# Kernel tuning notes

Hardware: AMD Instinct MI355X
Metric: run time of the kernel (lower is better)

The kernel has to match this reference:

```python
import jax, jax.numpy as jnp
import numpy as np

TEMPERATURE = 0.5
EPS = 1e-8  # matches F.cosine_similarity eps clamp


def setup_inputs() -> dict:
    key = jax.random.key(0)
    k1, k2 = jax.random.split(key)
    logits = jax.random.normal(k1, (8192, 256), dtype=jnp.float32)
    label = jax.random.randint(k2, (8192,), 0, 10, dtype=jnp.int64)
    return {"logits": logits, "label": label}


def reference(logits, label):
    n = label.shape[0]
    # pairwise cosine similarity via normalize + GEMM (same math as the
    # broadcasted F.cosine_similarity, without the O(n^2 d) intermediate)
    norms = jnp.maximum(jnp.linalg.norm(logits, axis=1, keepdims=True), EPS)
    xn = logits / norms                       # [n, d]
    sim_matrix = xn @ xn.T                    # [n, n]

    eye = jnp.eye(n, dtype=sim_matrix.dtype)
    mask = (label[:, None] == label[None, :]).astype(sim_matrix.dtype)  # same-label (incl. diag)

    e = jnp.exp(sim_matrix / TEMPERATURE) * (1.0 - eye)  # zero diagonal
    sim = mask * e                            # same-label positives
    no_sim_sum = jnp.sum(e - sim, axis=1)     # [n] row sums of different-label terms
    sim_sum = sim + no_sim_sum[:, None]       # denominator per entry
    ratio = sim / sim_sum

    # zeros (different-label entries) get +1 via (1 - mask), diagonal gets +1 via eye -> -log(1) = 0
    loss_mat = -jnp.log((1.0 - mask) + ratio + eye)
    return jnp.sum(loss_mat) / (2 * n)
```

## Files before the change

### kernel.cpp

```cpp
#include <hip/hip_runtime.h>
#include <cstdint>
#include <cstddef>

typedef float  f32x4  __attribute__((ext_vector_type(4)));
typedef long long i64;
typedef unsigned char uchar;

#define N_ROWS 8192
#define KDIM   256
#define TEMP_INV 2.0f
#define LOG2E  1.4426950408889634f
#define EXPC   (TEMP_INV * LOG2E)

#define AS1 __attribute__((address_space(1)))
#define AS3 __attribute__((address_space(3)))

__global__ __launch_bounds__(256) void prep(const float* __restrict__ logits,
        const int* __restrict__ label, uchar* __restrict__ xn8,
        int* __restrict__ perm, int* __restrict__ labelPerm,
        int* __restrict__ classStart, int* __restrict__ cumTiles)
{
    __shared__ int lcnt[256][10];
    __shared__ int cstart[11];
    __shared__ int ccount[10];
    const int tid = threadIdx.x;
    const int bid = blockIdx.x;

    if (bid < 2048) {
        const int p = bid * 4 + (tid >> 6);
        const int lane = tid & 63;
        float4 v = reinterpret_cast<const float4*>(logits + (size_t)p * KDIM)[lane];
        float ss = v.x*v.x + v.y*v.y + v.z*v.z + v.w*v.w;
        #pragma unroll
        for (int off = 32; off >= 1; off >>= 1) ss += __shfl_xor(ss, off, 64);
        float inv = 1.0f / fmaxf(sqrtf(ss), 1e-8f);
        int pk = __builtin_amdgcn_cvt_pk_fp8_f32(v.x * inv, v.y * inv, 0, false);
        pk     = __builtin_amdgcn_cvt_pk_fp8_f32(v.z * inv, v.w * inv, pk, true);
        reinterpret_cast<unsigned int*>(xn8 + (size_t)p * KDIM)[lane] = (unsigned int)pk;
        return;
    }

    const int wave = tid >> 6, lane = tid & 63;
    const int beg = tid * 32, end = beg + 32;
    int loc[10] = {0,0,0,0,0,0,0,0,0,0};
    for (int i = beg; i < end; ++i) {
        int c = label[i]; c = (c < 0) ? 0 : (c > 9 ? 9 : c);
        loc[c]++;
    }
    #pragma unroll
    for (int c = 0; c < 10; ++c) lcnt[tid][c] = loc[c];
    __syncthreads();

    for (int c = wave; c < 10; c += 4) {
        int s0 = lcnt[lane*4+0][c], s1 = lcnt[lane*4+1][c];
        int s2 = lcnt[lane*4+2][c], s3 = lcnt[lane*4+3][c];
        int tot = s0 + s1 + s2 + s3;
        int incl = tot;
        #pragma unroll
        for (int d = 1; d < 64; d <<= 1) {
            int up = __shfl_up(incl, d, 64);
            if (lane >= d) incl += up;
        }
        int excl = incl - tot;
        lcnt[lane*4+0][c] = excl;
        lcnt[lane*4+1][c] = excl + s0;
        lcnt[lane*4+2][c] = excl + s0 + s1;
        lcnt[lane*4+3][c] = excl + s0 + s1 + s2;
        if (lane == 63) ccount[c] = incl;
    }
    __syncthreads();

    if (tid == 0) {
        int run = 0, runT = 0;
        for (int c = 0; c < 10; ++c) {
            cstart[c] = run; classStart[c] = run;
            int tpc = (ccount[c] + 127) >> 7;
            cumTiles[c] = runT;
            run  += ccount[c];
            runT += tpc * (tpc + 1) / 2;
        }
        cstart[10] = run; classStart[10] = run; cumTiles[10] = runT;
    }
    __syncthreads();

    int ofs[10];
    #pragma unroll
    for (int c = 0; c < 10; ++c) ofs[c] = lcnt[tid][c];
    for (int i = beg; i < end; ++i) {
        int c = label[i]; c = (c < 0) ? 0 : (c > 9 ? 9 : c);
        int pos = cstart[c] + ofs[c]++;
        perm[pos] = i;
        labelPerm[pos] = c;
    }
}

__device__ __forceinline__ void stage_oneshot(const uchar* __restrict__ xn8,
        const int* __restrict__ perm, int rowBase, int colBase,
        uchar* As, uchar* Bs, int tid)
{
    const int t4 = tid >> 4;
    const int ch = (tid & 15) ^ t4;
    #pragma unroll
    for (int i = 0; i < 8; ++i) {
        const int row = i * 16 + t4;
        int rA = rowBase + row; if (rA > N_ROWS - 1) rA = N_ROWS - 1;
        int rB = colBase + row; if (rB > N_ROWS - 1) rB = N_ROWS - 1;
        const int lds_off = (i * 256 + tid) * 16;
        const uchar* gA = xn8 + (size_t)perm[rA] * KDIM + ch * 16;
        const uchar* gB = xn8 + (size_t)perm[rB] * KDIM + ch * 16;
        __builtin_amdgcn_global_load_lds((const AS1 void*)gA, (AS3 void*)(As + lds_off), 16, 0, 0);
        __builtin_amdgcn_global_load_lds((const AS1 void*)gB, (AS3 void*)(Bs + lds_off), 16, 0, 0);
    }
}

__device__ __forceinline__ void mfma_oneshot(const uchar* As, const uchar* Bs,
        f32x4 (&acc)[4][4], int wave, int lane)
{
    const int wr = wave >> 1, wc = wave & 1;
    const int lrow = lane & 15, kgrp = lane >> 4;
    const int ch2 = kgrp >> 1, half8 = (kgrp & 1) * 8;
    #pragma unroll
    for (int s = 0; s < 8; ++s) {
        const int c16 = s * 2 + ch2;
        i64 a[4], b[4];
        #pragma unroll
        for (int mi = 0; mi < 4; ++mi) {
            const int row = wr*64 + mi*16 + lrow;
            a[mi] = *reinterpret_cast<const i64*>(As + (size_t)row * 256 + ((c16 ^ lrow) * 16) + half8);
        }
        #pragma unroll
        for (int ni = 0; ni < 4; ++ni) {
            const int row = wc*64 + ni*16 + lrow;
            b[ni] = *reinterpret_cast<const i64*>(Bs + (size_t)row * 256 + ((c16 ^ lrow) * 16) + half8);
        }
        #pragma unroll
        for (int mi = 0; mi < 4; ++mi)
            #pragma unroll
            for (int ni = 0; ni < 4; ++ni)
                acc[mi][ni] = __builtin_amdgcn_mfma_f32_16x16x32_fp8_fp8(a[mi], b[ni], acc[mi][ni], 0, 0, 0);
    }
}

__global__ __launch_bounds__(256, 2) void phase1_gemm(const uchar* __restrict__ xn8,
        const int* __restrict__ perm, const int* __restrict__ labelPerm,
        float* __restrict__ pD)
{
    __shared__ __align__(16) char pool[65536];
    uchar* As = (uchar*)(pool);
    uchar* Bs = (uchar*)(pool + 32768);
    float* rowD = (float*)pool;
    float* colD = (float*)(pool + 16384);
    __shared__ int labLDS[256];

    const int tid = threadIdx.x;
    const int wave = tid >> 6, lane = tid & 63;

    int t = blockIdx.x, bi = 0;
    while (t >= 64 - bi) { t -= 64 - bi; ++bi; }
    const int bj = bi + t;
    const bool isDiag = (bi == bj);
    const int rowBase = bi * 128, colBase = bj * 128;

    if (labelPerm[rowBase] == labelPerm[colBase + 127]) {
        if (tid < 128)       pD[(size_t)bj * N_ROWS + rowBase + tid] = 0.f;
        else if (!isDiag)    pD[(size_t)bi * N_ROWS + colBase + tid - 128] = 0.f;
        return;
    }

    stage_oneshot(xn8, perm, rowBase, colBase, As, Bs, tid);
    labLDS[tid] = labelPerm[(tid < 128) ? (rowBase + tid) : (colBase + tid - 128)];
    __syncthreads();

    f32x4 acc[4][4] = {};
    mfma_oneshot(As, Bs, acc, wave, lane);
    __syncthreads();

    const int wr = wave >> 1, wc = wave & 1;
    const int lrow = lane & 15, lgrp = lane >> 4;
    float colAcc[4] = {0.f, 0.f, 0.f, 0.f};
    #pragma unroll
    for (int mi = 0; mi < 4; ++mi) {
        #pragma unroll
        for (int reg = 0; reg < 4; ++reg) {
            const int tr = wr * 64 + mi * 16 + lgrp * 4 + reg;
            const int rl = labLDS[tr];
            float rowAcc = 0.f;
            #pragma unroll
            for (int ni = 0; ni < 4; ++ni) {
                const int tc = wc * 64 + ni * 16 + lrow;
                float e = __builtin_amdgcn_exp2f(acc[mi][ni][reg] * EXPC);
                float ed = (rl != labLDS[128 + tc]) ? e : 0.f;
                rowAcc += ed;
                colAcc[ni] += ed;
            }
            rowD[tr * 32 + wc * 16 + lrow] = rowAcc;
        }
    }
    if (!isDiag) {
        #pragma unroll
        for (int ni = 0; ni < 4; ++ni) {
            const int tc = wc * 64 + ni * 16 + lrow;
            colD[tc * 8 + wr * 4 + lgrp] = colAcc[ni];
        }
    }
    __syncthreads();

    if (tid < 128) {
        const float* p = rowD + tid * 32;
        float s = 0.f;
        #pragma unroll
        for (int k = 0; k < 8; ++k) {
            f32x4 v = *reinterpret_cast<const f32x4*>(p + k * 4);
            s += v[0] + v[1] + v[2] + v[3];
        }
        pD[(size_t)bj * N_ROWS + rowBase + tid] = s;
    } else if (!isDiag) {
        const int c2 = tid - 128;
        const float* p = colD + c2 * 8;
        f32x4 v0 = *reinterpret_cast<const f32x4*>(p);
        f32x4 v1 = *reinterpret_cast<const f32x4*>(p + 4);
        pD[(size_t)bi * N_ROWS + colBase + c2] =
            v0[0] + v0[1] + v0[2] + v0[3] + v1[0] + v1[1] + v1[2] + v1[3];
    }
}

__global__ __launch_bounds__(256, 2) void phase3_loss(const uchar* __restrict__ xn8,
        const int* __restrict__ perm, const float* __restrict__ pD,
        const int* __restrict__ classStart, const int* __restrict__ cumTiles,
        float* __restrict__ partial)
{
    __shared__ __align__(16) char pool[65536];
    uchar* As = (uchar*)(pool);
    uchar* Bs = (uchar*)(pool + 32768);
    __shared__ float redF[256];
    __shared__ float DarrH[256];
    __shared__ float DarrR[128];
    __shared__ float DarrC[128];
    __shared__ int   meta[22];

    const int tid = threadIdx.x;
    const int wave = tid >> 6, lane = tid & 63;

    if (tid < 11) { meta[tid] = classStart[tid]; meta[11 + tid] = cumTiles[tid]; }
    __syncthreads();
    const int nTiles = meta[11 + 10];

    float tileSum = 0.f;
    for (int b = blockIdx.x; b < nTiles; b += 512) {
        __syncthreads();

        int c = 0;
        while (c < 9 && b >= meta[11 + c + 1]) ++c;
        const int s = meta[c], e = meta[c + 1];
        const int nc = e - s;
        const int tps = (nc + 127) >> 7;
        int lt = b - meta[11 + c];
        int ti = 0;
        while (lt >= tps - ti) { lt -= tps - ti; ++ti; }
        const int tj = ti + lt;
        const bool isDiagT = (ti == tj);
        const int rowBase = s + ti * 128, colBase = s + tj * 128;

        stage_oneshot(xn8, perm, rowBase, colBase, As, Bs, tid);

        {
            int r = rowBase + (tid & 127); if (r > N_ROWS - 1) r = N_ROWS - 1;
            const int half = tid >> 7;
            float d = 0.f;
            #pragma unroll 4
            for (int sl = half * 32; sl < half * 32 + 32; ++sl)
                d += pD[(size_t)sl * N_ROWS + r];
            DarrH[(tid & 127) * 2 + half] = d;
        }
        __syncthreads();
        if (tid < 128) DarrR[tid] = DarrH[tid * 2] + DarrH[tid * 2 + 1];
        __syncthreads();
        if (!isDiagT) {
            int r = colBase + (tid & 127); if (r > N_ROWS - 1) r = N_ROWS - 1;
            const int half = tid >> 7;
            float d = 0.f;
            #pragma unroll 4
            for (int sl = half * 32; sl < half * 32 + 32; ++sl)
                d += pD[(size_t)sl * N_ROWS + r];
            DarrH[(tid & 127) * 2 + half] = d;
            __syncthreads();
            if (tid < 128) DarrC[tid] = DarrH[tid * 2] + DarrH[tid * 2 + 1];
        }
        __syncthreads();

        f32x4 acc[4][4] = {};
        mfma_oneshot(As, Bs, acc, wave, lane);

        const int wr = wave >> 1, wc = wave & 1;
        const int lrow = lane & 15, lgrp = lane >> 4;
        #pragma unroll
        for (int mi = 0; mi < 4; ++mi) {
            #pragma unroll
            for (int reg = 0; reg < 4; ++reg) {
                const int tr = wr * 64 + mi * 16 + lgrp * 4 + reg;
                const int r = rowBase + tr;
                if (r < e) {
                    const float Dr = DarrR[tr];
                    #pragma unroll
                    for (int ni = 0; ni < 4; ++ni) {
                        const int tc = wc * 64 + ni * 16 + lrow;
                        const int cg = colBase + tc;
                        if (cg < e) {
                            float sim = acc[mi][ni][reg];
                            float ev = __builtin_amdgcn_exp2f(sim * EXPC);
                            if (isDiagT) {
                                if (cg != r)
                                    tileSum += __logf(ev + Dr) - TEMP_INV * sim;
                            } else {
                                tileSum += __logf(ev + Dr) + __logf(ev + DarrC[tc])
                                         - 2.0f * TEMP_INV * sim;
                            }
                        }
                    }
                }
            }
        }
    }

    __syncthreads();
    redF[tid] = tileSum;
    __syncthreads();
    for (int st = 128; st > 0; st >>= 1) {
        if (tid < st) redF[tid] += redF[tid + st];
        __syncthreads();
    }
    if (tid == 0) partial[blockIdx.x] = redF[0];
}

__global__ void phase4_final(const float* __restrict__ partial, float* __restrict__ out)
{
    __shared__ float red[256];
    const int tid = threadIdx.x;
    float s = partial[tid] + partial[tid + 256];
    red[tid] = s;
    __syncthreads();
    for (int st = 128; st > 0; st >>= 1) {
        if (tid < st) red[tid] += red[tid + st];
        __syncthreads();
    }
    if (tid == 0) out[0] = red[0] * (1.0f / 16384.0f);
}

extern "C" void kernel_launch(void* const* d_in, const int* in_sizes, int n_in,
                              void* d_out, int out_size, void* d_ws, size_t ws_size,
                              hipStream_t stream)
{
    const float* logits = (const float*)d_in[0];
    const int*   label  = (const int*)d_in[1];
    float* out = (float*)d_out;

    char* ws = (char*)d_ws;
    uchar*  xn8       = (uchar*)(ws);
    float*  pD        = (float*)(ws + (2u << 20));
    int*    perm      = (int*)(ws + (4u << 20));
    int*    labelPerm = (int*)(ws + (4u << 20) + (32u << 10));
    int*    classStart= (int*)(ws + (4u << 20) + (64u << 10));
    int*    cumTiles  = (int*)(ws + (4u << 20) + (64u << 10) + 256);
    float*  partial   = (float*)(ws + (4u << 20) + (128u << 10));

    hipLaunchKernelGGL(prep, dim3(2049), dim3(256), 0, stream,
                       logits, label, xn8, perm, labelPerm, classStart, cumTiles);
    hipLaunchKernelGGL(phase1_gemm, dim3(2080), dim3(256), 0, stream,
                       xn8, perm, labelPerm, pD);
    hipLaunchKernelGGL(phase3_loss, dim3(512), dim3(256), 0, stream,
                       xn8, perm, pD, classStart, cumTiles, partial);
    hipLaunchKernelGGL(phase4_final, dim3(1), dim3(256), 0, stream,
                       partial, out);
}
```

Before: 67.97 us.

## Use 512-thread blocks in phase1 GEMM and coalesce label scan in prep

phase1_gemm now runs 8 waves per 128x128 tile, each computing a 64x32 sub-tile, so each wave holds fewer accumulators and there are more waves per tile to hide latency. Row and column partial sums are reduced with cross-lane shuffles before being written to LDS, which shrinks the final reduction. The prep kernel reads labels strided by thread (coalesced) into registers once, instead of each thread reading a contiguous 32-element run twice. The risk is that 512-thread blocks with 64KB of LDS limit how many blocks fit per CU, and the extra shuffles add instructions. The permutation order within each class also changes.

```diff
diff --git a/kernel.cpp b/kernel.cpp
--- a/kernel.cpp
+++ b/kernel.cpp
@@ -41,12 +41,15 @@
     }
 
     const int wave = tid >> 6, lane = tid & 63;
-    const int beg = tid * 32, end = beg + 32;
+    int lab[32];
+    #pragma unroll
+    for (int j = 0; j < 32; ++j) {
+        int c = label[tid + j * 256];
+        lab[j] = (c < 0) ? 0 : (c > 9 ? 9 : c);
+    }
     int loc[10] = {0,0,0,0,0,0,0,0,0,0};
-    for (int i = beg; i < end; ++i) {
-        int c = label[i]; c = (c < 0) ? 0 : (c > 9 ? 9 : c);
-        loc[c]++;
-    }
+    #pragma unroll
+    for (int j = 0; j < 32; ++j) loc[lab[j]]++;
     #pragma unroll
     for (int c = 0; c < 10; ++c) lcnt[tid][c] = loc[c];
     __syncthreads();
@@ -86,11 +89,125 @@
     int ofs[10];
     #pragma unroll
     for (int c = 0; c < 10; ++c) ofs[c] = lcnt[tid][c];
-    for (int i = beg; i < end; ++i) {
-        int c = label[i]; c = (c < 0) ? 0 : (c > 9 ? 9 : c);
+    #pragma unroll
+    for (int j = 0; j < 32; ++j) {
+        int c = lab[j];
         int pos = cstart[c] + ofs[c]++;
-        perm[pos] = i;
+        perm[pos] = tid + j * 256;
         labelPerm[pos] = c;
+    }
+}
+
+__global__ __launch_bounds__(512, 4) void phase1_gemm(const uchar* __restrict__ xn8,
+        const int* __restrict__ perm, const int* __restrict__ labelPerm,
+        float* __restrict__ pD)
+{
+    __shared__ __align__(16) char pool[65536];
+    uchar* As = (uchar*)(pool);
+    uchar* Bs = (uchar*)(pool + 32768);
+    float* rowD = (float*)pool;
+    float* colD = (float*)(pool + 32768);
+    __shared__ int labLDS[256];
+
+    const int tid = threadIdx.x;
+    const int wave = tid >> 6, lane = tid & 63;
+
+    int t = blockIdx.x, bi = 0;
+    while (t >= 64 - bi) { t -= 64 - bi; ++bi; }
+    const int bj = bi + t;
+    const bool isDiag = (bi == bj);
+    const int rowBase = bi * 128, colBase = bj * 128;
+
+    if (labelPerm[rowBase] == labelPerm[colBase + 127]) {
+        if (tid < 128)                    pD[(size_t)bj * N_ROWS + rowBase + tid] = 0.f;
+        else if (tid < 256 && !isDiag)    pD[(size_t)bi * N_ROWS + colBase + tid - 128] = 0.f;
+        return;
+    }
+
+    {
+        const int t4 = (tid >> 4) & 15;
+        const int ch = (tid & 15) ^ t4;
+        #pragma unroll
+        for (int i = 0; i < 4; ++i) {
+            const int ci = i * 512 + tid;
+            const int row = ci >> 4;
+            const int lds_off = ci * 16;
+            const uchar* gA = xn8 + (size_t)perm[rowBase + row] * KDIM + ch * 16;
+            const uchar* gB = xn8 + (size_t)perm[colBase + row] * KDIM + ch * 16;
+            __builtin_amdgcn_global_load_lds((const AS1 void*)gA, (AS3 void*)(As + lds_off), 16, 0, 0);
+            __builtin_amdgcn_global_load_lds((const AS1 void*)gB, (AS3 void*)(Bs + lds_off), 16, 0, 0);
+        }
+    }
+    if (tid < 256)
+        labLDS[tid] = labelPerm[(tid < 128) ? (rowBase + tid) : (colBase + tid - 128)];
+    __syncthreads();
+
+    const int wr = wave >> 2, wc = wave & 3;
+    const int lrow = lane & 15, kgrp = lane >> 4;
+    const int ch2 = kgrp >> 1, half8 = (kgrp & 1) * 8;
+    f32x4 acc[4][2] = {};
+    #pragma unroll
+    for (int s = 0; s < 8; ++s) {
+        const int c16 = s * 2 + ch2;
+        i64 a[4], b[2];
+        #pragma unroll
+        for (int mi = 0; mi < 4; ++mi) {
+            const int row = wr*64 + mi*16 + lrow;
+            a[mi] = *reinterpret_cast<const i64*>(As + (size_t)row * 256 + ((c16 ^ lrow) * 16) + half8);
+        }
+        #pragma unroll
+        for (int ni = 0; ni < 2; ++ni) {
+            const int row = wc*32 + ni*16 + lrow;
+            b[ni] = *reinterpret_cast<const i64*>(Bs + (size_t)row * 256 + ((c16 ^ lrow) * 16) + half8);
+        }
+        #pragma unroll
+        for (int mi = 0; mi < 4; ++mi)
+            #pragma unroll
+            for (int ni = 0; ni < 2; ++ni)
+                acc[mi][ni] = __builtin_amdgcn_mfma_f32_16x16x32_fp8_fp8(a[mi], b[ni], acc[mi][ni], 0, 0, 0);
+    }
+    __syncthreads();
+
+    const int lgrp = lane >> 4;
+    float colAcc[2] = {0.f, 0.f};
+    #pragma unroll
+    for (int mi = 0; mi < 4; ++mi) {
+        #pragma unroll
+        for (int reg = 0; reg < 4; ++reg) {
+            const int tr = wr * 64 + mi * 16 + lgrp * 4 + reg;
+            const int rl = labLDS[tr];
+            float rowAcc = 0.f;
+            #pragma unroll
+            for (int ni = 0; ni < 2; ++ni) {
+                const int tc = wc * 32 + ni * 16 + lrow;
+                float e = __builtin_amdgcn_exp2f(acc[mi][ni][reg] * EXPC);
+                float ed = (rl != labLDS[128 + tc]) ? e : 0.f;
+                rowAcc += ed;
+                colAcc[ni] += ed;
+            }
+            #pragma unroll
+            for (int off = 1; off < 16; off <<= 1)
+                rowAcc += __shfl_xor(rowAcc, off, 64);
+            if (lrow == 0) rowD[tr * 4 + wc] = rowAcc;
+        }
+    }
+    #pragma unroll
+    for (int ni = 0; ni < 2; ++ni) {
+        colAcc[ni] += __shfl_xor(colAcc[ni], 16, 64);
+        colAcc[ni] += __shfl_xor(colAcc[ni], 32, 64);
+        if (lgrp == 0) {
+            const int tc = wc * 32 + ni * 16 + lrow;
+            colD[tc * 2 + wr] = colAcc[ni];
+        }
+    }
+    __syncthreads();
+
+    if (tid < 128) {
+        pD[(size_t)bj * N_ROWS + rowBase + tid] =
+            rowD[tid * 4] + rowD[tid * 4 + 1] + rowD[tid * 4 + 2] + rowD[tid * 4 + 3];
+    } else if (tid < 256 && !isDiag) {
+        const int c2 = tid - 128;
+        pD[(size_t)bi * N_ROWS + colBase + c2] = colD[c2 * 2] + colD[c2 * 2 + 1];
     }
 }
 
@@ -138,89 +255,6 @@
             #pragma unroll
             for (int ni = 0; ni < 4; ++ni)
                 acc[mi][ni] = __builtin_amdgcn_mfma_f32_16x16x32_fp8_fp8(a[mi], b[ni], acc[mi][ni], 0, 0, 0);
-    }
-}
-
-__global__ __launch_bounds__(256, 2) void phase1_gemm(const uchar* __restrict__ xn8,
-        const int* __restrict__ perm, const int* __restrict__ labelPerm,
-        float* __restrict__ pD)
-{
-    __shared__ __align__(16) char pool[65536];
-    uchar* As = (uchar*)(pool);
-    uchar* Bs = (uchar*)(pool + 32768);
-    float* rowD = (float*)pool;
-    float* colD = (float*)(pool + 16384);
-    __shared__ int labLDS[256];
-
-    const int tid = threadIdx.x;
-    const int wave = tid >> 6, lane = tid & 63;
-
-    int t = blockIdx.x, bi = 0;
-    while (t >= 64 - bi) { t -= 64 - bi; ++bi; }
-    const int bj = bi + t;
-    const bool isDiag = (bi == bj);
-    const int rowBase = bi * 128, colBase = bj * 128;
-
-    if (labelPerm[rowBase] == labelPerm[colBase + 127]) {
-        if (tid < 128)       pD[(size_t)bj * N_ROWS + rowBase + tid] = 0.f;
-        else if (!isDiag)    pD[(size_t)bi * N_ROWS + colBase + tid - 128] = 0.f;
-        return;
-    }
-
-    stage_oneshot(xn8, perm, rowBase, colBase, As, Bs, tid);
-    labLDS[tid] = labelPerm[(tid < 128) ? (rowBase + tid) : (colBase + tid - 128)];
-    __syncthreads();
-
-    f32x4 acc[4][4] = {};
-    mfma_oneshot(As, Bs, acc, wave, lane);
-    __syncthreads();
-
-    const int wr = wave >> 1, wc = wave & 1;
-    const int lrow = lane & 15, lgrp = lane >> 4;
-    float colAcc[4] = {0.f, 0.f, 0.f, 0.f};
-    #pragma unroll
-    for (int mi = 0; mi < 4; ++mi) {
-        #pragma unroll
-        for (int reg = 0; reg < 4; ++reg) {
-            const int tr = wr * 64 + mi * 16 + lgrp * 4 + reg;
-            const int rl = labLDS[tr];
-            float rowAcc = 0.f;
-            #pragma unroll
-            for (int ni = 0; ni < 4; ++ni) {
-                const int tc = wc * 64 + ni * 16 + lrow;
-                float e = __builtin_amdgcn_exp2f(acc[mi][ni][reg] * EXPC);
-                float ed = (rl != labLDS[128 + tc]) ? e : 0.f;
-                rowAcc += ed;
-                colAcc[ni] += ed;
-            }
-            rowD[tr * 32 + wc * 16 + lrow] = rowAcc;
-        }
-    }
-    if (!isDiag) {
-        #pragma unroll
-        for (int ni = 0; ni < 4; ++ni) {
-            const int tc = wc * 64 + ni * 16 + lrow;
-            colD[tc * 8 + wr * 4 + lgrp] = colAcc[ni];
-        }
-    }
-    __syncthreads();
-
-    if (tid < 128) {
-        const float* p = rowD + tid * 32;
-        float s = 0.f;
-        #pragma unroll
-        for (int k = 0; k < 8; ++k) {
-            f32x4 v = *reinterpret_cast<const f32x4*>(p + k * 4);
-            s += v[0] + v[1] + v[2] + v[3];
-        }
-        pD[(size_t)bj * N_ROWS + rowBase + tid] = s;
-    } else if (!isDiag) {
-        const int c2 = tid - 128;
-        const float* p = colD + c2 * 8;
-        f32x4 v0 = *reinterpret_cast<const f32x4*>(p);
-        f32x4 v1 = *reinterpret_cast<const f32x4*>(p + 4);
-        pD[(size_t)bi * N_ROWS + colBase + c2] =
-            v0[0] + v0[1] + v0[2] + v0[3] + v1[0] + v1[1] + v1[2] + v1[3];
     }
 }
 
@@ -365,7 +399,7 @@
 
     hipLaunchKernelGGL(prep, dim3(2049), dim3(256), 0, stream,
                        logits, label, xn8, perm, labelPerm, classStart, cumTiles);
-    hipLaunchKernelGGL(phase1_gemm, dim3(2080), dim3(256), 0, stream,
+    hipLaunchKernelGGL(phase1_gemm, dim3(2080), dim3(512), 0, stream,
                        xn8, perm, labelPerm, pD);
     hipLaunchKernelGGL(phase3_loss, dim3(512), dim3(256), 0, stream,
                        xn8, perm, pD, classStart, cumTiles, partial);
```

Measured after the change: 76.35 us. 1.12x slower.

## Skip duplicate B staging on diagonal tiles, coalesce label reads, memset partial buffer

Applied to the files above, without the earlier changes.

On diagonal tiles, both GEMM kernels now stage only the A operand and reuse it as B, which halves global-to-LDS traffic for those tiles. The label scan in prep switches to strided, coalesced loads held in registers instead of reading each thread's contiguous chunk twice. Fully same-label tiles in phase1 now return early without zeroing pD, and an added hipMemsetAsync of pD covers that. The memset is an extra launch and a 2 MB write that may cost more than it saves.

```diff
diff --git a/kernel.cpp b/kernel.cpp
--- a/kernel.cpp
+++ b/kernel.cpp
@@ -41,12 +41,15 @@
     }
 
     const int wave = tid >> 6, lane = tid & 63;
-    const int beg = tid * 32, end = beg + 32;
+    int lab[32];
+    #pragma unroll
+    for (int j = 0; j < 32; ++j) {
+        int c = label[tid + j * 256];
+        lab[j] = (c < 0) ? 0 : (c > 9 ? 9 : c);
+    }
     int loc[10] = {0,0,0,0,0,0,0,0,0,0};
-    for (int i = beg; i < end; ++i) {
-        int c = label[i]; c = (c < 0) ? 0 : (c > 9 ? 9 : c);
-        loc[c]++;
-    }
+    #pragma unroll
+    for (int j = 0; j < 32; ++j) loc[lab[j]]++;
     #pragma unroll
     for (int c = 0; c < 10; ++c) lcnt[tid][c] = loc[c];
     __syncthreads();
@@ -86,30 +89,27 @@
     int ofs[10];
     #pragma unroll
     for (int c = 0; c < 10; ++c) ofs[c] = lcnt[tid][c];
-    for (int i = beg; i < end; ++i) {
-        int c = label[i]; c = (c < 0) ? 0 : (c > 9 ? 9 : c);
+    #pragma unroll
+    for (int j = 0; j < 32; ++j) {
+        int c = lab[j];
         int pos = cstart[c] + ofs[c]++;
-        perm[pos] = i;
+        perm[pos] = tid + j * 256;
         labelPerm[pos] = c;
     }
 }
 
-__device__ __forceinline__ void stage_oneshot(const uchar* __restrict__ xn8,
-        const int* __restrict__ perm, int rowBase, int colBase,
-        uchar* As, uchar* Bs, int tid)
+__device__ __forceinline__ void stage_mat(const uchar* __restrict__ xn8,
+        const int* __restrict__ perm, int base, uchar* dst, int tid)
 {
     const int t4 = tid >> 4;
     const int ch = (tid & 15) ^ t4;
     #pragma unroll
     for (int i = 0; i < 8; ++i) {
         const int row = i * 16 + t4;
-        int rA = rowBase + row; if (rA > N_ROWS - 1) rA = N_ROWS - 1;
-        int rB = colBase + row; if (rB > N_ROWS - 1) rB = N_ROWS - 1;
+        int r = base + row; if (r > N_ROWS - 1) r = N_ROWS - 1;
         const int lds_off = (i * 256 + tid) * 16;
-        const uchar* gA = xn8 + (size_t)perm[rA] * KDIM + ch * 16;
-        const uchar* gB = xn8 + (size_t)perm[rB] * KDIM + ch * 16;
-        __builtin_amdgcn_global_load_lds((const AS1 void*)gA, (AS3 void*)(As + lds_off), 16, 0, 0);
-        __builtin_amdgcn_global_load_lds((const AS1 void*)gB, (AS3 void*)(Bs + lds_off), 16, 0, 0);
+        const uchar* g = xn8 + (size_t)perm[r] * KDIM + ch * 16;
+        __builtin_amdgcn_global_load_lds((const AS1 void*)g, (AS3 void*)(dst + lds_off), 16, 0, 0);
     }
 }
 
@@ -161,18 +161,16 @@
     const bool isDiag = (bi == bj);
     const int rowBase = bi * 128, colBase = bj * 128;
 
-    if (labelPerm[rowBase] == labelPerm[colBase + 127]) {
-        if (tid < 128)       pD[(size_t)bj * N_ROWS + rowBase + tid] = 0.f;
-        else if (!isDiag)    pD[(size_t)bi * N_ROWS + colBase + tid - 128] = 0.f;
-        return;
-    }
-
-    stage_oneshot(xn8, perm, rowBase, colBase, As, Bs, tid);
+    if (labelPerm[rowBase] == labelPerm[colBase + 127]) return;
+
+    stage_mat(xn8, perm, rowBase, As, tid);
+    if (!isDiag) stage_mat(xn8, perm, colBase, Bs, tid);
+    const uchar* Bsrc = isDiag ? As : Bs;
     labLDS[tid] = labelPerm[(tid < 128) ? (rowBase + tid) : (colBase + tid - 128)];
     __syncthreads();
 
     f32x4 acc[4][4] = {};
-    mfma_oneshot(As, Bs, acc, wave, lane);
+    mfma_oneshot(As, Bsrc, acc, wave, lane);
     __syncthreads();
 
     const int wr = wave >> 1, wc = wave & 1;
@@ -261,7 +259,9 @@
         const bool isDiagT = (ti == tj);
         const int rowBase = s + ti * 128, colBase = s + tj * 128;
 
-        stage_oneshot(xn8, perm, rowBase, colBase, As, Bs, tid);
+        stage_mat(xn8, perm, rowBase, As, tid);
+        if (!isDiagT) stage_mat(xn8, perm, colBase, Bs, tid);
+        const uchar* Bsrc = isDiagT ? As : Bs;
 
         {
             int r = rowBase + (tid & 127); if (r > N_ROWS - 1) r = N_ROWS - 1;
@@ -289,7 +289,7 @@
         __syncthreads();
 
         f32x4 acc[4][4] = {};
-        mfma_oneshot(As, Bs, acc, wave, lane);
+        mfma_oneshot(As, Bsrc, acc, wave, lane);
 
         const int wr = wave >> 1, wc = wave & 1;
         const int lrow = lane & 15, lgrp = lane >> 4;
@@ -363,6 +363,7 @@
     int*    cumTiles  = (int*)(ws + (4u << 20) + (64u << 10) + 256);
     float*  partial   = (float*)(ws + (4u << 20) + (128u << 10));
 
+    hipMemsetAsync(pD, 0, (size_t)64 * N_ROWS * sizeof(float), stream);
     hipLaunchKernelGGL(prep, dim3(2049), dim3(256), 0, stream,
                        logits, label, xn8, perm, labelPerm, classStart, cumTiles);
     hipLaunchKernelGGL(phase1_gemm, dim3(2080), dim3(256), 0, stream,
```

After: 72.14 us. 6.1% more time.
